# Kernel tuning notes

Measured on AMD Instinct MI355X. Metric: run time of the kernel, lower is better.

## Reference

```python
import jax, jax.numpy as jnp
import numpy as np

# int64 needed: torch does the prime-multiply hash in int64 (products ~1e13 overflow int32)
jax.config.update("jax_enable_x64", True)

NUM_LEVELS = 16
LEVEL_DIM = 2
HASH_SIZE = 2 ** 19
INPUT_DIM = 3
N_POINTS = 2_097_152

_b = (2048 / 16) ** (1.0 / (NUM_LEVELS - 1))
RESOLUTIONS = np.array([int(16 * _b ** i) for i in range(NUM_LEVELS)], dtype=np.float32)  # [L]
PRIMES = np.array([1, 2654435761, 805459861], dtype=np.int64)[:INPUT_DIM]  # [3]


def setup_inputs() -> dict:
    key = jax.random.key(0)
    kx, ke = jax.random.split(key)
    x = jax.random.uniform(kx, (N_POINTS, INPUT_DIM), dtype=jnp.float32)  # coords in [0,1)
    # nn.init.uniform_(emb.weight, -1e-4, 1e-4), stacked across the 16 levels
    embeddings = jax.random.uniform(
        ke, (NUM_LEVELS, HASH_SIZE, LEVEL_DIM), dtype=jnp.float32, minval=-1e-4, maxval=1e-4
    )
    return {"x": x, "embeddings": embeddings}


def reference(x, embeddings):
    # x: [N, 3] float32; embeddings: [L, HS, D] float32
    res = jnp.asarray(RESOLUTIONS)                      # [L]
    primes = jnp.asarray(PRIMES)                        # [3] int64
    # all levels at once: [L, N, 3]
    x_floor = jnp.floor(x[None, :, :] * res[:, None, None]).astype(jnp.int64)
    hash_idx = (x_floor * primes).sum(axis=-1) % HASH_SIZE  # [L, N] int64
    # per-level gather: [L, N, D]
    feats = jax.vmap(lambda table, idx: table[idx])(embeddings, hash_idx)
    # concat levels along feature dim -> [N, L*D]
    n = x.shape[0]
    return jnp.transpose(feats, (1, 0, 2)).reshape(n, NUM_LEVELS * LEVEL_DIM)
```

## Files before the change

### kernel.cpp

```cpp
#include <hip/hip_runtime.h>
#include <math.h>

#define HASH_SIZE_LOG2 19
#define HASH_MASK ((1u << HASH_SIZE_LOG2) - 1u)
#define HS (1u << HASH_SIZE_LOG2)
#define NUM_LEVELS 16
#define CHUNK 2048

typedef float f32x2 __attribute__((ext_vector_type(2)));
typedef float f32x4 __attribute__((ext_vector_type(4)));

struct ResArr { float r[NUM_LEVELS]; };

__global__ __launch_bounds__(256) void he_gather_kernel(
    const float* __restrict__ x,
    const float* __restrict__ emb,
    f32x2* __restrict__ ws,
    ResArr res, int n_points, int chunks)
{
    __shared__ float sx[CHUNK * 3];

    const int bid = blockIdx.x;
    const int seg = bid / (8 * chunks);
    const int r   = bid - seg * 8 * chunks;
    const int lvl = seg * 8 + (r & 7);
    const int chunk = r >> 3;
    const long long base = (long long)chunk * CHUNK;
    const int t = threadIdx.x;

    const f32x4* x4 = (const f32x4*)x;
    const long long nflt4 = ((long long)n_points * 3) / 4;
    for (int i = t; i < CHUNK * 3 / 4; i += 256) {
        long long gi = (long long)chunk * (CHUNK * 3 / 4) + i;
        f32x4 v = (gi < nflt4) ? __builtin_nontemporal_load(&x4[gi])
                               : (f32x4){0, 0, 0, 0};
        ((f32x4*)sx)[i] = v;
    }
    __syncthreads();

    const float rl = res.r[lvl];
    const f32x2* __restrict__ table = (const f32x2*)emb + (size_t)lvl * HS;
    f32x2* __restrict__ wsl = ws + (size_t)lvl * n_points;
    const unsigned P1 = 2654435761u, P2 = 805459861u;

    unsigned h[8];
    #pragma unroll
    for (int j = 0; j < 8; j++) {
        const int p = t + j * 256;
        unsigned c0 = (unsigned)(int)floorf(sx[p * 3 + 0] * rl);
        unsigned c1 = (unsigned)(int)floorf(sx[p * 3 + 1] * rl);
        unsigned c2 = (unsigned)(int)floorf(sx[p * 3 + 2] * rl);
        h[j] = (c0 + c1 * P1 + c2 * P2) & HASH_MASK;
    }
    f32x2 f[8];
    #pragma unroll
    for (int j = 0; j < 8; j++) f[j] = table[h[j]];
    #pragma unroll
    for (int j = 0; j < 8; j++) {
        const long long n = base + t + j * 256;
        if (n < n_points) __builtin_nontemporal_store(f[j], &wsl[n]);
    }
}

__global__ __launch_bounds__(256) void he_transpose_kernel(
    const f32x2* __restrict__ ws, float* __restrict__ out, int n_points)
{
    __shared__ f32x2 sf[256 * 17];
    const long long base = (long long)blockIdx.x * 256;
    const int t = threadIdx.x;
    const long long n = base + t;

    #pragma unroll
    for (int l = 0; l < NUM_LEVELS; l++) {
        f32x2 v = (n < n_points)
            ? __builtin_nontemporal_load(&ws[(size_t)l * n_points + n])
            : (f32x2){0, 0};
        sf[t * 17 + l] = v;
    }
    __syncthreads();

    #pragma unroll
    for (int j = 0; j < 8; j++) {
        const int i = t + j * 256;
        const int p = i >> 3;
        const int c2 = (i & 7) * 2;
        if (base + p < n_points) {
            f32x2 a = sf[p * 17 + c2];
            f32x2 b = sf[p * 17 + c2 + 1];
            f32x4 v = {a.x, a.y, b.x, b.y};
            __builtin_nontemporal_store(v, (f32x4*)out + (base * 8 + i));
        }
    }
}

__global__ __launch_bounds__(256) void he_direct_kernel(
    const float* __restrict__ x, const float* __restrict__ emb,
    float* __restrict__ out, ResArr res, int n_points)
{
    __shared__ float sx[128 * 3];
    __shared__ float sres[NUM_LEVELS];
    const int t = threadIdx.x;
    const long long base = (long long)blockIdx.x * 128;
    if (t < NUM_LEVELS) sres[t] = res.r[t];
    for (int i = t; i < 384; i += 256) {
        long long gi = base * 3 + i;
        sx[i] = (gi < (long long)n_points * 3)
                    ? __builtin_nontemporal_load(&x[gi]) : 0.0f;
    }
    __syncthreads();
    const int lp = t & 7, pl = t >> 3, l0 = lp * 2;
    const float rA = sres[l0], rB = sres[l0 + 1];
    const unsigned P1 = 2654435761u, P2 = 805459861u;
    const f32x2* __restrict__ e2 = (const f32x2*)emb;
    unsigned ha[4], hb[4];
    #pragma unroll
    for (int j = 0; j < 4; j++) {
        const int pj = pl + j * 32;
        const float x0 = sx[pj * 3], x1 = sx[pj * 3 + 1], x2 = sx[pj * 3 + 2];
        unsigned a0 = (unsigned)(int)floorf(x0 * rA);
        unsigned a1 = (unsigned)(int)floorf(x1 * rA);
        unsigned a2 = (unsigned)(int)floorf(x2 * rA);
        unsigned b0 = (unsigned)(int)floorf(x0 * rB);
        unsigned b1 = (unsigned)(int)floorf(x1 * rB);
        unsigned b2 = (unsigned)(int)floorf(x2 * rB);
        ha[j] = (a0 + a1 * P1 + a2 * P2) & HASH_MASK;
        hb[j] = (b0 + b1 * P1 + b2 * P2) & HASH_MASK;
    }
    f32x2 fa[4], fb[4];
    #pragma unroll
    for (int j = 0; j < 4; j++) {
        fa[j] = e2[(size_t)l0 * HS + ha[j]];
        fb[j] = e2[((size_t)l0 + 1) * HS + hb[j]];
    }
    #pragma unroll
    for (int j = 0; j < 4; j++) {
        const long long n = base + pl + j * 32;
        if (n < n_points) {
            f32x4 v = {fa[j].x, fa[j].y, fb[j].x, fb[j].y};
            __builtin_nontemporal_store(v, (f32x4*)out + (n * 8 + lp));
        }
    }
}

extern "C" void kernel_launch(void* const* d_in, const int* in_sizes, int n_in,
                              void* d_out, int out_size, void* d_ws, size_t ws_size,
                              hipStream_t stream) {
    const float* x   = (const float*)d_in[0];
    const float* emb = (const float*)d_in[1];
    float* out = (float*)d_out;
    const int n = in_sizes[0] / 3;

    ResArr res;
    const double b = pow(128.0, 1.0 / 15.0);
    for (int i = 0; i < NUM_LEVELS; i++) {
        res.r[i] = (float)(long long)(16.0 * pow(b, (double)i));
    }

    const size_t ws_need = (size_t)NUM_LEVELS * (size_t)n * sizeof(f32x2);
    if (ws_size >= ws_need) {
        const int chunks = (n + CHUNK - 1) / CHUNK;
        he_gather_kernel<<<2 * 8 * chunks, 256, 0, stream>>>(
            x, emb, (f32x2*)d_ws, res, n, chunks);
        he_transpose_kernel<<<(n + 255) / 256, 256, 0, stream>>>(
            (const f32x2*)d_ws, out, n);
    } else {
        he_direct_kernel<<<(n + 127) / 128, 256, 0, stream>>>(x, emb, out, res, n);
    }
}
```

Measured before the change: 351.7 us.

## Schedule gather blocks across XCDs by level and point octant for L2 locality

Replaces the simple level/chunk block mapping with a host-built schedule table that assigns each XCD (block id mod 8) a set of (level, point-octant) work slots. The coarse levels 0-4 are spread evenly over the XCDs, and the eleven large-table levels 5-15 are split into octants so that each XCD's L2 sees a limited set of hash tables. The aim is better L2 hit rates on the random table gathers. It relies on blocks being dispatched round-robin across XCDs and adds an early-exit branch for padded chunks.

```diff
diff --git a/kernel.cpp b/kernel.cpp
--- a/kernel.cpp
+++ b/kernel.cpp
@@ -12,19 +12,29 @@
 
 struct ResArr { float r[NUM_LEVELS]; };
 
+struct Sched {
+    unsigned char lvl[128];
+    unsigned char oct[128];
+    ResArr res;
+};
+
 __global__ __launch_bounds__(256) void he_gather_kernel(
     const float* __restrict__ x,
     const float* __restrict__ emb,
     f32x2* __restrict__ ws,
-    ResArr res, int n_points, int chunks)
+    Sched sc, int n_points, int ochunks, int chunks)
 {
     __shared__ float sx[CHUNK * 3];
 
     const int bid = blockIdx.x;
-    const int seg = bid / (8 * chunks);
-    const int r   = bid - seg * 8 * chunks;
-    const int lvl = seg * 8 + (r & 7);
-    const int chunk = r >> 3;
+    const int xcd = bid & 7;
+    const int r = bid >> 3;
+    const int slot = r / ochunks;
+    const int c = r - slot * ochunks;
+    const int lvl = sc.lvl[xcd * 16 + slot];
+    const int chunk = (int)sc.oct[xcd * 16 + slot] * ochunks + c;
+    if (chunk >= chunks) return;
+
     const long long base = (long long)chunk * CHUNK;
     const int t = threadIdx.x;
 
@@ -38,7 +48,7 @@
     }
     __syncthreads();
 
-    const float rl = res.r[lvl];
+    const float rl = sc.res.r[lvl];
     const f32x2* __restrict__ table = (const f32x2*)emb + (size_t)lvl * HS;
     f32x2* __restrict__ wsl = ws + (size_t)lvl * n_points;
     const unsigned P1 = 2654435761u, P2 = 805459861u;
@@ -158,9 +168,22 @@
 
     const size_t ws_need = (size_t)NUM_LEVELS * (size_t)n * sizeof(f32x2);
     if (ws_size >= ws_need) {
+        Sched sc;
+        sc.res = res;
+        for (int q = 0; q < 88; q++) {
+            int xcd = q / 11, slot = q % 11;
+            sc.lvl[xcd * 16 + slot] = (unsigned char)(5 + q / 8);
+            sc.oct[xcd * 16 + slot] = (unsigned char)(q % 8);
+        }
+        for (int s = 0; s < 40; s++) {
+            int xcd = s / 5, slot = 11 + s % 5;
+            sc.lvl[xcd * 16 + slot] = (unsigned char)(s / 8);
+            sc.oct[xcd * 16 + slot] = (unsigned char)(s % 8);
+        }
         const int chunks = (n + CHUNK - 1) / CHUNK;
-        he_gather_kernel<<<2 * 8 * chunks, 256, 0, stream>>>(
-            x, emb, (f32x2*)d_ws, res, n, chunks);
+        const int ochunks = (chunks + 7) / 8;
+        he_gather_kernel<<<8 * 16 * ochunks, 256, 0, stream>>>(
+            x, emb, (f32x2*)d_ws, sc, n, ochunks, chunks);
         he_transpose_kernel<<<(n + 255) / 256, 256, 0, stream>>>(
             (const f32x2*)d_ws, out, n);
     } else {
```

Result: faster. 342.4 us (-2.7%).
